# Kernel tuning notes

Hardware: AMD Instinct MI355X
Metric: run time of the kernel (lower is better)

## Reference

```python
import jax, jax.numpy as jnp
import numpy as np

SQ, SK, B, NP, HN = 2048, 2048, 2, 32, 64

def setup_inputs() -> dict:
    key = jax.random.key(0)
    kq, kk, kv, km = jax.random.split(key, 4)
    query = jax.random.normal(kq, (SQ, B, NP, HN), dtype=jnp.float32)
    k = jax.random.normal(kk, (SK, B, NP, HN), dtype=jnp.float32)
    value = jax.random.normal(kv, (SK, B, NP, HN), dtype=jnp.float32)
    # True = masked position (matches tf.where(mask, -10000.0, scores));
    # use a causal-style mask broadcast over heads.
    causal = ~jnp.tril(jnp.ones((SQ, SK), dtype=bool))  # True above diagonal
    attention_mask = jnp.broadcast_to(causal[None, None], (B, 1, SQ, SK))
    return {"query": query, "key": k, "value": value, "attention_mask": attention_mask}

def reference(query, key, value, attention_mask):
    sq, b, nh, hn = query.shape
    norm_factor = jnp.sqrt(jnp.asarray(hn, dtype=query.dtype))
    # scores: [b, nh, sq, sk]
    scores = jnp.einsum('sbnh,tbnh->bnst', query, key) / norm_factor
    scores = jnp.where(attention_mask, jnp.asarray(-10000.0, scores.dtype), scores)
    probs = jax.nn.softmax(scores, axis=-1)
    # dropout rate is 0.0 / inference -> identity
    # context: [sq, b, nh, hn] -> [sq, b, nh*hn]
    context = jnp.einsum('bnst,tbnh->sbnh', probs, value)
    return context.reshape(sq, b, nh * hn)
```

## Files before the change

### kernel.cpp

```cpp
#include <hip/hip_runtime.h>


typedef __attribute__((ext_vector_type(8))) short frag8;
typedef __attribute__((ext_vector_type(4))) float f32x4;

#define SQ_    2048
#define NH_    64
#define HN_    64
#define ROWS_  4096
#define P_P    40
#define VT_P   40
#define TP_    72
#define SC2    (0.125f * 1.44269504088896340736f)
#define MASK2  (-3.0e4f)
#define MINIT  (-1.0e30f)

__device__ __forceinline__ unsigned short f2bf(float f) {
    unsigned u = __float_as_uint(f);
    u += 0x7fffu + ((u >> 16) & 1u);
    return (unsigned short)(u >> 16);
}

__device__ __forceinline__ float fexp2(float x) {
#if __has_builtin(__builtin_amdgcn_exp2f)
    return __builtin_amdgcn_exp2f(x);
#else
    return exp2f(x);
#endif
}

__device__ __forceinline__ frag8 pack8s(const float* __restrict__ p, float s) {
    float4 a = *(const float4*)p;
    float4 b = *(const float4*)(p + 4);
    frag8 r;
    r[0] = (short)f2bf(a.x * s); r[1] = (short)f2bf(a.y * s);
    r[2] = (short)f2bf(a.z * s); r[3] = (short)f2bf(a.w * s);
    r[4] = (short)f2bf(b.x * s); r[5] = (short)f2bf(b.y * s);
    r[6] = (short)f2bf(b.z * s); r[7] = (short)f2bf(b.w * s);
    return r;
}

__device__ __forceinline__ void gll(const void* g, void* l) {
    __builtin_amdgcn_global_load_lds(
        (const __attribute__((address_space(1))) unsigned int*)(uintptr_t)g,
        (__attribute__((address_space(3))) unsigned int*)(unsigned int)(uintptr_t)l,
        16, 0, 0);
}

__global__ void __launch_bounds__(256)
prep_kv(const float* __restrict__ K, const float* __restrict__ V,
        unsigned short* __restrict__ Kh, unsigned short* __restrict__ Vblk)
{
    __shared__ __align__(16) unsigned short tile[HN_ * TP_];
    const int tid = threadIdx.x;
    const int hd  = blockIdx.x & 63;
    const int s0  = (blockIdx.x >> 6) << 6;

    {
        const int c2 = tid & 3;
        const int sl = tid >> 2;
        const int s  = s0 + sl;
        const float* kp = K + (size_t)s * ROWS_ + hd * HN_ + c2 * 16;
        frag8 A = pack8s(kp, 1.0f);
        frag8 Bf = pack8s(kp + 8, 1.0f);
        unsigned short* kr = Kh + (size_t)hd * (SQ_ * HN_) + (size_t)s * HN_;
        *(frag8*)(kr + ((2 * c2 + s) & 7) * 8)     = A;
        *(frag8*)(kr + ((2 * c2 + 1 + s) & 7) * 8) = Bf;
    }

    {
        const int c   = (tid & 15) * 4;
        const int tl0 = tid >> 4;
#pragma unroll
        for (int k = 0; k < 4; ++k) {
            const int tl = tl0 + k * 16;
            float4 v = *(const float4*)(V + (size_t)(s0 + tl) * ROWS_ + hd * HN_ + c);
            tile[(c + 0) * TP_ + tl] = f2bf(v.x);
            tile[(c + 1) * TP_ + tl] = f2bf(v.y);
            tile[(c + 2) * TP_ + tl] = f2bf(v.z);
            tile[(c + 3) * TP_ + tl] = f2bf(v.w);
        }
    }
    __syncthreads();
    {
        const int u  = tid & 3;
        const int dd = tid >> 2;
        const int rv = (dd + (dd >> 1)) & 3;
#pragma unroll
        for (int tb = 0; tb < 2; ++tb) {
            frag8 r = *(const frag8*)&tile[dd * TP_ + tb * 32 + u * 8];
            unsigned short* vr = Vblk + ((size_t)hd * 64 + (s0 >> 5) + tb) * 2048 + dd * 32;
            *(frag8*)(vr + ((u + rv) & 3) * 8) = r;
        }
    }
}

template <bool MASKED>
__device__ __forceinline__ void
ctile(const unsigned short* __restrict__ Kl, const unsigned short* __restrict__ Vl,
      int t0, int rowBase, int quad, int ln,
      const frag8& aq0, const frag8& aq1,
      unsigned short* __restrict__ PlW, f32x4 acc[4], float l_part[4])
{
    const int sw0 = ((quad + ln) & 7) * 8;
    const int sw1 = ((quad + 4 + ln) & 7) * 8;
    frag8 bk00 = *(const frag8*)(Kl + ln * 64 + sw0);
    frag8 bk01 = *(const frag8*)(Kl + ln * 64 + sw1);
    frag8 bk10 = *(const frag8*)(Kl + (16 + ln) * 64 + sw0);
    frag8 bk11 = *(const frag8*)(Kl + (16 + ln) * 64 + sw1);

    f32x4 c0 = (f32x4){0.f, 0.f, 0.f, 0.f};
    f32x4 c1 = (f32x4){0.f, 0.f, 0.f, 0.f};
    c0 = __builtin_amdgcn_mfma_f32_16x16x32_bf16(aq0, bk00, c0, 0, 0, 0);
    c0 = __builtin_amdgcn_mfma_f32_16x16x32_bf16(aq1, bk01, c0, 0, 0, 0);
    c1 = __builtin_amdgcn_mfma_f32_16x16x32_bf16(aq0, bk10, c1, 0, 0, 0);
    c1 = __builtin_amdgcn_mfma_f32_16x16x32_bf16(aq1, bk11, c1, 0, 0, 0);

#pragma unroll
    for (int r = 0; r < 4; ++r) {
        float p0 = fexp2(c0[r]);
        float p1 = fexp2(c1[r]);
        if (MASKED) {
            const int row = rowBase + quad * 4 + r;
            p0 = (t0 + ln > row)      ? 0.f : p0;
            p1 = (t0 + 16 + ln > row) ? 0.f : p1;
        }
        l_part[r] += p0 + p1;
        PlW[(quad * 4 + r) * P_P + ln]      = f2bf(p0);
        PlW[(quad * 4 + r) * P_P + 16 + ln] = f2bf(p1);
    }

    const int rv = (ln + (ln >> 1)) & 3;
    const int swv = ((quad + rv) & 3) * 8;
    frag8 bv0 = *(const frag8*)(Vl + (0 * 16 + ln) * 32 + swv);
    frag8 bv1 = *(const frag8*)(Vl + (1 * 16 + ln) * 32 + swv);
    frag8 bv2 = *(const frag8*)(Vl + (2 * 16 + ln) * 32 + swv);
    frag8 bv3 = *(const frag8*)(Vl + (3 * 16 + ln) * 32 + swv);

    asm volatile("s_waitcnt lgkmcnt(0)" ::: "memory");
    frag8 ap = *(const frag8*)&PlW[ln * P_P + quad * 8];
    acc[0] = __builtin_amdgcn_mfma_f32_16x16x32_bf16(ap, bv0, acc[0], 0, 0, 0);
    acc[1] = __builtin_amdgcn_mfma_f32_16x16x32_bf16(ap, bv1, acc[1], 0, 0, 0);
    acc[2] = __builtin_amdgcn_mfma_f32_16x16x32_bf16(ap, bv2, acc[2], 0, 0, 0);
    acc[3] = __builtin_amdgcn_mfma_f32_16x16x32_bf16(ap, bv3, acc[3], 0, 0, 0);
}

__global__ void __launch_bounds__(256, 6)
attn_fwd3(const float* __restrict__ Qg,
          const unsigned short* __restrict__ Kh,
          const unsigned short* __restrict__ Vblk,
          float* __restrict__ Og)
{
    __shared__ __align__(16) unsigned short sbuf[2][4096];
    __shared__ __align__(16) unsigned short Pl[4][16 * P_P];

    const int tid  = threadIdx.x;
    const int wave = tid >> 6;
    const int lane = tid & 63;
    const int quad = lane >> 4;
    const int ln   = lane & 15;

    const int hd = blockIdx.x & 63;
    const int qt = 31 - (blockIdx.x >> 6);
    const int rowBase = qt * 64 + wave * 16;
    const int t0p  = rowBase & ~31;
    const int tiles = 2 * qt + 2;

    frag8 aq0, aq1;
    {
        const float* qp = Qg + (size_t)(rowBase + ln) * ROWS_ + hd * HN_ + quad * 8;
        aq0 = pack8s(qp, SC2);
        aq1 = pack8s(qp + 32, SC2);
    }

    f32x4 acc[4];
    float l_part[4];
#pragma unroll
    for (int r = 0; r < 4; ++r) {
        l_part[r] = 0.f;
        acc[r] = (f32x4){0.f, 0.f, 0.f, 0.f};
    }

    const unsigned short* khHead = Kh   + (size_t)hd * (SQ_ * HN_);
    const unsigned short* vbHead = Vblk + (size_t)hd * 64 * 2048;
    unsigned short* PlW = &Pl[wave][0];

    const int koff = (wave < 2) ? wave * 2048 : (wave - 2) * 2048;
    const int doff = (wave < 2) ? koff : 4096 + koff;

    {
        const char* src = (wave < 2) ? ((const char*)khHead) : ((const char*)vbHead);
        const char* s = src + koff + lane * 16;
        char* d = (char*)&sbuf[0][0] + doff;
        gll(s, d);
        gll(s + 1024, d + 1024);
    }

    for (int t = 0; t < tiles; ++t) {
        asm volatile("s_barrier" ::: "memory");
        {
            const int tn = (t + 1 < tiles) ? t + 1 : t;
            const char* src = (wave < 2) ? ((const char*)(khHead + (size_t)tn * 2048))
                                         : ((const char*)(vbHead + (size_t)tn * 2048));
            const char* s = src + koff + lane * 16;
            char* d = (char*)&sbuf[(t + 1) & 1][0] + doff;
            gll(s, d);
            gll(s + 1024, d + 1024);
        }
        asm volatile("s_waitcnt vmcnt(2)" ::: "memory");
        asm volatile("s_barrier" ::: "memory");

        const int t0 = t * 32;
        const unsigned short* Kl = &sbuf[t & 1][0];
        const unsigned short* Vl = &sbuf[t & 1][2048];
        if (t0 < t0p)
            ctile<false>(Kl, Vl, t0, rowBase, quad, ln, aq0, aq1, PlW, acc, l_part);
        else if (t0 == t0p)
            ctile<true>(Kl, Vl, t0, rowBase, quad, ln, aq0, aq1, PlW, acc, l_part);
    }
    asm volatile("s_waitcnt vmcnt(0)" ::: "memory");

#pragma unroll
    for (int r = 0; r < 4; ++r) {
        float l = l_part[r];
        l += __shfl_xor(l, 1);
        l += __shfl_xor(l, 2);
        l += __shfl_xor(l, 4);
        l += __shfl_xor(l, 8);
        const float inv = 1.0f / l;
        float* op = Og + (size_t)(rowBase + quad * 4 + r) * ROWS_ + hd * HN_ + ln;
        op[0]  = acc[0][r] * inv;
        op[16] = acc[1][r] * inv;
        op[32] = acc[2][r] * inv;
        op[48] = acc[3][r] * inv;
    }
}

__global__ void __launch_bounds__(256)
attn_fwd(const float* __restrict__ Qg, const float* __restrict__ Kg,
         const float* __restrict__ Vg, float* __restrict__ Og)
{
    __shared__ __align__(16) unsigned short Vt[HN_ * VT_P];
    __shared__ __align__(16) unsigned short Pl[4][16 * P_P];
    const int tid  = threadIdx.x;
    const int wave = tid >> 6;
    const int lane = tid & 63;
    const int quad = lane >> 4;
    const int ln   = lane & 15;
    const int hd = blockIdx.x % NH_;
    const int qt = 31 - (blockIdx.x / NH_);
    const int q0 = qt * 64;
    const int rowBase = q0 + wave * 16;
    frag8 aq0, aq1;
    {
        const float* qp = Qg + (size_t)(rowBase + ln) * ROWS_ + hd * HN_ + quad * 8;
        aq0 = pack8s(qp, 1.0f);
        aq1 = pack8s(qp + 32, 1.0f);
    }
    f32x4 acc[4];
    float m_i[4], l_i[4];
#pragma unroll
    for (int r = 0; r < 4; ++r) {
        m_i[r] = MINIT; l_i[r] = 0.f;
        acc[r] = (f32x4){0.f, 0.f, 0.f, 0.f};
    }
    const int tEnd = q0 + 64;
    for (int t0 = 0; t0 < tEnd; t0 += 32) {
        __syncthreads();
        {
            const int t  = tid >> 3;
            const int dc = tid & 7;
            const float* vp = Vg + (size_t)(t0 + t) * ROWS_ + hd * HN_ + dc * 8;
            float4 v0 = *(const float4*)vp;
            float4 v1 = *(const float4*)(vp + 4);
            Vt[(dc * 8 + 0) * VT_P + t] = f2bf(v0.x);
            Vt[(dc * 8 + 1) * VT_P + t] = f2bf(v0.y);
            Vt[(dc * 8 + 2) * VT_P + t] = f2bf(v0.z);
            Vt[(dc * 8 + 3) * VT_P + t] = f2bf(v0.w);
            Vt[(dc * 8 + 4) * VT_P + t] = f2bf(v1.x);
            Vt[(dc * 8 + 5) * VT_P + t] = f2bf(v1.y);
            Vt[(dc * 8 + 6) * VT_P + t] = f2bf(v1.z);
            Vt[(dc * 8 + 7) * VT_P + t] = f2bf(v1.w);
        }
        __syncthreads();
        float s0[4], s1[4];
#pragma unroll
        for (int sub = 0; sub < 2; ++sub) {
            const float* kp = Kg + (size_t)(t0 + sub * 16 + ln) * ROWS_ + hd * HN_ + quad * 8;
            frag8 bk0 = pack8s(kp, 1.0f);
            frag8 bk1 = pack8s(kp + 32, 1.0f);
            f32x4 c = (f32x4){0.f, 0.f, 0.f, 0.f};
            c = __builtin_amdgcn_mfma_f32_16x16x32_bf16(aq0, bk0, c, 0, 0, 0);
            c = __builtin_amdgcn_mfma_f32_16x16x32_bf16(aq1, bk1, c, 0, 0, 0);
            const int col = t0 + sub * 16 + ln;
            float* dst = sub ? s1 : s0;
#pragma unroll
            for (int r = 0; r < 4; ++r) {
                const int row = rowBase + quad * 4 + r;
                dst[r] = (col > row) ? MASK2 : c[r] * SC2;
            }
        }
#pragma unroll
        for (int r = 0; r < 4; ++r) {
            float mx = fmaxf(s0[r], s1[r]);
            mx = fmaxf(mx, __shfl_xor(mx, 1));
            mx = fmaxf(mx, __shfl_xor(mx, 2));
            mx = fmaxf(mx, __shfl_xor(mx, 4));
            mx = fmaxf(mx, __shfl_xor(mx, 8));
            const float mnew  = fmaxf(m_i[r], mx);
            const float alpha = fexp2(m_i[r] - mnew);
            const float p0 = fexp2(s0[r] - mnew);
            const float p1 = fexp2(s1[r] - mnew);
            float rs = p0 + p1;
            rs += __shfl_xor(rs, 1);
            rs += __shfl_xor(rs, 2);
            rs += __shfl_xor(rs, 4);
            rs += __shfl_xor(rs, 8);
            l_i[r] = l_i[r] * alpha + rs;
            m_i[r] = mnew;
#pragma unroll
            for (int dc = 0; dc < 4; ++dc) acc[dc][r] *= alpha;
            Pl[wave][(quad * 4 + r) * P_P + ln]      = f2bf(p0);
            Pl[wave][(quad * 4 + r) * P_P + 16 + ln] = f2bf(p1);
        }
        asm volatile("s_waitcnt lgkmcnt(0)" ::: "memory");
        frag8 ap = *(const frag8*)&Pl[wave][ln * P_P + quad * 8];
#pragma unroll
        for (int dc = 0; dc < 4; ++dc) {
            frag8 bv = *(const frag8*)&Vt[(dc * 16 + ln) * VT_P + quad * 8];
            acc[dc] = __builtin_amdgcn_mfma_f32_16x16x32_bf16(ap, bv, acc[dc], 0, 0, 0);
        }
    }
#pragma unroll
    for (int r = 0; r < 4; ++r) {
        const float inv = 1.0f / l_i[r];
        float* op = Og + (size_t)(rowBase + quad * 4 + r) * ROWS_ + hd * HN_ + ln;
#pragma unroll
        for (int dc = 0; dc < 4; ++dc)
            op[dc * 16] = acc[dc][r] * inv;
    }
}

extern "C" void kernel_launch(void* const* d_in, const int* in_sizes, int n_in,
                              void* d_out, int out_size, void* d_ws, size_t ws_size,
                              hipStream_t stream) {
    const float* Q = (const float*)d_in[0];
    const float* K = (const float*)d_in[1];
    const float* V = (const float*)d_in[2];
    float* O = (float*)d_out;

    const size_t HALF = (size_t)SQ_ * ROWS_ * sizeof(unsigned short);
    if (ws_size >= 2 * HALF) {
        unsigned short* Kh   = (unsigned short*)d_ws;
        unsigned short* Vblk = (unsigned short*)((char*)d_ws + HALF);
        prep_kv<<<dim3(NH_ * (SQ_ / 64)), dim3(256), 0, stream>>>(K, V, Kh, Vblk);
        attn_fwd3<<<dim3(2048), dim3(256), 0, stream>>>(Q, Kh, Vblk, O);
    } else {
        attn_fwd<<<dim3(2048), dim3(256), 0, stream>>>(Q, K, V, O);
    }
}
```

Baseline: 206.3 us.

## Stage 64-key tiles per barrier, swizzle V transpose tile, cheaper bf16 rounding

The attention kernel now loads 64 keys of K and V per double-buffer stage instead of 32, running two 32-key sub-tiles per iteration. This halves the number of barriers and loop iterations, and the diagonal tile handles masking per wave. The change doubles shared memory per block and lowers the occupancy hint from 6 to 4. prep_kv rotates columns in the V transpose tile to cut LDS bank conflicts, and probability rounding to bf16 drops the round-to-nearest-even step in favour of a plain add.

```diff
diff --git a/kernel.cpp b/kernel.cpp
--- a/kernel.cpp
+++ b/kernel.cpp
@@ -9,11 +9,8 @@
 #define HN_    64
 #define ROWS_  4096
 #define P_P    40
-#define VT_P   40
 #define TP_    72
 #define SC2    (0.125f * 1.44269504088896340736f)
-#define MASK2  (-3.0e4f)
-#define MINIT  (-1.0e30f)
 
 __device__ __forceinline__ unsigned short f2bf(float f) {
     unsigned u = __float_as_uint(f);
@@ -61,7 +58,7 @@
         const int sl = tid >> 2;
         const int s  = s0 + sl;
         const float* kp = K + (size_t)s * ROWS_ + hd * HN_ + c2 * 16;
-        frag8 A = pack8s(kp, 1.0f);
+        frag8 A  = pack8s(kp, 1.0f);
         frag8 Bf = pack8s(kp + 8, 1.0f);
         unsigned short* kr = Kh + (size_t)hd * (SQ_ * HN_) + (size_t)s * HN_;
         *(frag8*)(kr + ((2 * c2 + s) & 7) * 8)     = A;
@@ -69,26 +66,31 @@
     }
 
     {
-        const int c   = (tid & 15) * 4;
-        const int tl0 = tid >> 4;
+        const int cIdx = tid & 15;
+        const int c    = cIdx * 4;
+        const int tl0  = tid >> 4;
+        const int rot  = (cIdx & 7) * 8;
 #pragma unroll
         for (int k = 0; k < 4; ++k) {
-            const int tl = tl0 + k * 16;
+            const int tl  = tl0 + k * 16;
+            const int col = (tl + rot) & 63;
             float4 v = *(const float4*)(V + (size_t)(s0 + tl) * ROWS_ + hd * HN_ + c);
-            tile[(c + 0) * TP_ + tl] = f2bf(v.x);
-            tile[(c + 1) * TP_ + tl] = f2bf(v.y);
-            tile[(c + 2) * TP_ + tl] = f2bf(v.z);
-            tile[(c + 3) * TP_ + tl] = f2bf(v.w);
+            tile[(c + 0) * TP_ + col] = f2bf(v.x);
+            tile[(c + 1) * TP_ + col] = f2bf(v.y);
+            tile[(c + 2) * TP_ + col] = f2bf(v.z);
+            tile[(c + 3) * TP_ + col] = f2bf(v.w);
         }
     }
     __syncthreads();
     {
         const int u  = tid & 3;
         const int dd = tid >> 2;
+        const int g  = (dd >> 2) & 7;
         const int rv = (dd + (dd >> 1)) & 3;
 #pragma unroll
         for (int tb = 0; tb < 2; ++tb) {
-            frag8 r = *(const frag8*)&tile[dd * TP_ + tb * 32 + u * 8];
+            const int sc = (tb * 4 + u + g) & 7;
+            frag8 r = *(const frag8*)&tile[dd * TP_ + sc * 8];
             unsigned short* vr = Vblk + ((size_t)hd * 64 + (s0 >> 5) + tb) * 2048 + dd * 32;
             *(frag8*)(vr + ((u + rv) & 3) * 8) = r;
         }
@@ -126,11 +128,13 @@
             p1 = (t0 + 16 + ln > row) ? 0.f : p1;
         }
         l_part[r] += p0 + p1;
-        PlW[(quad * 4 + r) * P_P + ln]      = f2bf(p0);
-        PlW[(quad * 4 + r) * P_P + 16 + ln] = f2bf(p1);
-    }
-
-    const int rv = (ln + (ln >> 1)) & 3;
+        const unsigned u0 = __float_as_uint(p0) + 0x8000u;
+        const unsigned u1 = __float_as_uint(p1) + 0x8000u;
+        PlW[(quad * 4 + r) * P_P + ln]      = (unsigned short)(u0 >> 16);
+        PlW[(quad * 4 + r) * P_P + 16 + ln] = (unsigned short)(u1 >> 16);
+    }
+
+    const int rv  = (ln + (ln >> 1)) & 3;
     const int swv = ((quad + rv) & 3) * 8;
     frag8 bv0 = *(const frag8*)(Vl + (0 * 16 + ln) * 32 + swv);
     frag8 bv1 = *(const frag8*)(Vl + (1 * 16 + ln) * 32 + swv);
@@ -145,13 +149,13 @@
     acc[3] = __builtin_amdgcn_mfma_f32_16x16x32_bf16(ap, bv3, acc[3], 0, 0, 0);
 }
 
-__global__ void __launch_bounds__(256, 6)
-attn_fwd3(const float* __restrict__ Qg,
+__global__ void __launch_bounds__(256, 4)
+attn_fwd4(const float* __restrict__ Qg,
           const unsigned short* __restrict__ Kh,
           const unsigned short* __restrict__ Vblk,
           float* __restrict__ Og)
 {
-    __shared__ __align__(16) unsigned short sbuf[2][4096];
+    __shared__ __align__(16) unsigned short sbuf[2][8192];
     __shared__ __align__(16) unsigned short Pl[4][16 * P_P];
 
     const int tid  = threadIdx.x;
@@ -163,8 +167,6 @@
     const int hd = blockIdx.x & 63;
     const int qt = 31 - (blockIdx.x >> 6);
     const int rowBase = qt * 64 + wave * 16;
-    const int t0p  = rowBase & ~31;
-    const int tiles = 2 * qt + 2;
 
     frag8 aq0, aq1;
     {
@@ -181,42 +183,45 @@
         acc[r] = (f32x4){0.f, 0.f, 0.f, 0.f};
     }
 
-    const unsigned short* khHead = Kh   + (size_t)hd * (SQ_ * HN_);
-    const unsigned short* vbHead = Vblk + (size_t)hd * 64 * 2048;
+    const char* khHead = (const char*)(Kh   + (size_t)hd * (SQ_ * HN_));
+    const char* vbHead = (const char*)(Vblk + (size_t)hd * 64 * 2048);
     unsigned short* PlW = &Pl[wave][0];
 
-    const int koff = (wave < 2) ? wave * 2048 : (wave - 2) * 2048;
-    const int doff = (wave < 2) ? koff : 4096 + koff;
-
-    {
-        const char* src = (wave < 2) ? ((const char*)khHead) : ((const char*)vbHead);
-        const char* s = src + koff + lane * 16;
+    const int half = (wave & 1) * 4096;
+    const int doff = (wave < 2) ? half : 8192 + half;
+
+    {
+        const char* s = ((wave < 2) ? khHead : vbHead) + half + lane * 16;
         char* d = (char*)&sbuf[0][0] + doff;
-        gll(s, d);
-        gll(s + 1024, d + 1024);
-    }
-
-    for (int t = 0; t < tiles; ++t) {
+        gll(s, d); gll(s + 1024, d + 1024);
+        gll(s + 2048, d + 2048); gll(s + 3072, d + 3072);
+    }
+
+    for (int t = 0; t <= qt; ++t) {
         asm volatile("s_barrier" ::: "memory");
         {
-            const int tn = (t + 1 < tiles) ? t + 1 : t;
-            const char* src = (wave < 2) ? ((const char*)(khHead + (size_t)tn * 2048))
-                                         : ((const char*)(vbHead + (size_t)tn * 2048));
-            const char* s = src + koff + lane * 16;
+            const int tn = (t < qt) ? t + 1 : t;
+            const char* s = ((wave < 2) ? khHead : vbHead) + (size_t)tn * 8192
+                            + half + lane * 16;
             char* d = (char*)&sbuf[(t + 1) & 1][0] + doff;
-            gll(s, d);
-            gll(s + 1024, d + 1024);
-        }
-        asm volatile("s_waitcnt vmcnt(2)" ::: "memory");
+            gll(s, d); gll(s + 1024, d + 1024);
+            gll(s + 2048, d + 2048); gll(s + 3072, d + 3072);
+        }
+        asm volatile("s_waitcnt vmcnt(4)" ::: "memory");
         asm volatile("s_barrier" ::: "memory");
 
-        const int t0 = t * 32;
         const unsigned short* Kl = &sbuf[t & 1][0];
-        const unsigned short* Vl = &sbuf[t & 1][2048];
-        if (t0 < t0p)
-            ctile<false>(Kl, Vl, t0, rowBase, quad, ln, aq0, aq1, PlW, acc, l_part);
-        else if (t0 == t0p)
-            ctile<true>(Kl, Vl, t0, rowBase, quad, ln, aq0, aq1, PlW, acc, l_part);
+        const unsigned short* Vl = &sbuf[t & 1][4096];
+        const int k0 = t * 64;
+        if (t < qt) {
+            ctile<false>(Kl,           Vl,        k0,      rowBase, quad, ln, aq0, aq1, PlW, acc, l_part);
+            ctile<false>(Kl + 32 * 64, Vl + 2048, k0 + 32, rowBase, quad, ln, aq0, aq1, PlW, acc, l_part);
+        } else if (wave < 2) {
+            ctile<true>(Kl, Vl, k0, rowBase, quad, ln, aq0, aq1, PlW, acc, l_part);
+        } else {
+            ctile<false>(Kl,           Vl,        k0,      rowBase, quad, ln, aq0, aq1, PlW, acc, l_part);
+            ctile<true>(Kl + 32 * 64,  Vl + 2048, k0 + 32, rowBase, quad, ln, aq0, aq1, PlW, acc, l_part);
+        }
     }
     asm volatile("s_waitcnt vmcnt(0)" ::: "memory");
 
@@ -236,6 +241,9 @@
     }
 }
 
+#define VT_P   40
+#define MASK2  (-3.0e4f)
+#define MINIT  (-1.0e30f)
 __global__ void __launch_bounds__(256)
 attn_fwd(const float* __restrict__ Qg, const float* __restrict__ Kg,
          const float* __restrict__ Vg, float* __restrict__ Og)
@@ -354,7 +362,7 @@
         unsigned short* Kh   = (unsigned short*)d_ws;
         unsigned short* Vblk = (unsigned short*)((char*)d_ws + HALF);
         prep_kv<<<dim3(NH_ * (SQ_ / 64)), dim3(256), 0, stream>>>(K, V, Kh, Vblk);
-        attn_fwd3<<<dim3(2048), dim3(256), 0, stream>>>(Q, Kh, Vblk, O);
+        attn_fwd4<<<dim3(2048), dim3(256), 0, stream>>>(Q, Kh, Vblk, O);
     } else {
         attn_fwd<<<dim3(2048), dim3(256), 0, stream>>>(Q, K, V, O);
     }
```

Result: no change. 210.1 us (+1.9%).
